# Kernel tuning notes

Hardware: AMD Instinct MI355X
Metric: run time of the kernel (lower is better)

The kernel has to match this reference:

```python
import jax, jax.numpy as jnp
import numpy as np

LAMBDA_COORD = 5.0
LAMBDA_NOOBJ = 0.5


def _iou(box1, box2):
    # boxes: [..., 4] in (cx, cy, w, h) format. Matches YoloLoss.IOU:
    # returns 0 when x_right < x_left or y_bottom < y_top (strict),
    # else intersection / (area1 + area2 - intersection).
    x1, y1, w1, h1 = box1[..., 0], box1[..., 1], box1[..., 2], box1[..., 3]
    x2, y2, w2, h2 = box2[..., 0], box2[..., 1], box2[..., 2], box2[..., 3]
    x_left = jnp.maximum(x1 - w1 / 2, x2 - w2 / 2)
    y_top = jnp.maximum(y1 - h1 / 2, y2 - h2 / 2)
    x_right = jnp.minimum(x1 + w1 / 2, x2 + w2 / 2)
    y_bottom = jnp.minimum(y1 + h1 / 2, y2 + h2 / 2)
    valid = jnp.logical_and(x_right >= x_left, y_bottom >= y_top)
    inter = (x_right - x_left) * (y_bottom - y_top)
    union = w1 * h1 + w2 * h2 - inter
    safe_union = jnp.where(union == 0, 1.0, union)
    return jnp.where(valid, inter / safe_union, 0.0)


def setup_inputs() -> dict:
    key = jax.random.key(0)
    k1, k2 = jax.random.split(key)
    B, S, D = 16384, 7, 30  # D = 2*5 + 20
    y = jax.random.normal(k1, (B, S, S, D), dtype=jnp.float32)
    gt = jax.random.normal(k2, (B, S, S, D), dtype=jnp.float32)
    return {"y": y, "gt": gt}


def reference(y, gt):
    pred, target = y, gt
    batch_size = pred.shape[0]
    obj = (target[..., 4] > 0).astype(pred.dtype)      # [B,S,S]
    noobj = (target[..., 4] == 0).astype(pred.dtype)   # [B,S,S]

    # class loss (mask over class channels, indices 10:)
    class_loss = jnp.sum(obj[..., None] * (target[..., 10:] - pred[..., 10:]) ** 2)

    # no-object confidence loss (channel 4, mask before responsibility edits)
    conf_loss_no_obj = jnp.sum(noobj * (target[..., 4] - pred[..., 4]) ** 2)

    # per-cell IOU of target box vs both predicted boxes
    tbox = target[..., 0:4]
    iou1 = _iou(tbox, pred[..., 0:4])   # [B,S,S]
    iou2 = _iou(tbox, pred[..., 5:9])   # [B,S,S]

    # responsibility: keep box1 iff iou1 > iou2 (ties -> box2), as in the torch loop
    resp1 = (iou1 > iou2).astype(pred.dtype)
    m1 = obj * resp1          # box1 responsible mask
    m2 = obj * (1.0 - resp1)  # box2 responsible mask

    # object confidence loss: confidence target is the IOU of the responsible box
    conf_loss_obj = jnp.sum(m1 * (iou1 - pred[..., 4]) ** 2
                            + m2 * (iou2 - pred[..., 9]) ** 2)

    # xy loss (channels 0,1 / 5,6)
    xy_loss = jnp.sum(m1 * ((target[..., 0] - pred[..., 0]) ** 2
                            + (target[..., 1] - pred[..., 1]) ** 2)
                      + m2 * ((target[..., 0] - pred[..., 5]) ** 2
                              + (target[..., 1] - pred[..., 6]) ** 2))

    # wh loss (channels 2,3 / 7,8)
    wh_loss = jnp.sum(m1 * ((target[..., 2] - pred[..., 2]) ** 2
                            + (target[..., 3] - pred[..., 3]) ** 2)
                      + m2 * ((target[..., 2] - pred[..., 7]) ** 2
                              + (target[..., 3] - pred[..., 8]) ** 2))

    total = (LAMBDA_COORD * xy_loss + LAMBDA_COORD * wh_loss
             + conf_loss_obj + LAMBDA_NOOBJ * conf_loss_no_obj
             + class_loss) / batch_size
    return total
```

## Files before the change

### kernel.cpp

```cpp
#include <hip/hip_runtime.h>

#define LAMBDA_COORD 5.0f
#define LAMBDA_NOOBJ 0.5f
#define DD 30
#define BLOCK 256
#define CPB 256
#define CHUNKS ((CPB * DD * 4) / 1024)

#define EL(A, k) (((k) & 1) ? A[(k) >> 1].y : A[(k) >> 1].x)

__device__ __forceinline__ float iou_t(float tx, float ty, float tw, float th,
                                       float px, float py, float pw, float ph) {
    float xl = fmaxf(tx - tw * 0.5f, px - pw * 0.5f);
    float yt = fmaxf(ty - th * 0.5f, py - ph * 0.5f);
    float xr = fminf(tx + tw * 0.5f, px + pw * 0.5f);
    float yb = fminf(ty + th * 0.5f, py + ph * 0.5f);
    bool valid = (xr >= xl) && (yb >= yt);
    float inter = (xr - xl) * (yb - yt);
    float uni = tw * th + pw * ph - inter;
    float safe = (uni == 0.0f) ? 1.0f : uni;
    return valid ? (inter / safe) : 0.0f;
}

__global__ __launch_bounds__(BLOCK, 2) void yolo_loss_kernel(
    const float* __restrict__ pred, const float* __restrict__ targ,
    float* __restrict__ out) {
    __shared__ __align__(16) float ldsP[CPB * DD];
    __shared__ __align__(16) float ldsT[CPB * DD];
    __shared__ float wpart[BLOCK / 64];

    const int tid  = threadIdx.x;
    const int lane = tid & 63;
    const int wv   = tid >> 6;

    const size_t base = (size_t)blockIdx.x * (CPB * DD);
    const float* gp = pred + base;
    const float* gt = targ + base;

    for (int s = wv; s < CHUNKS; s += BLOCK / 64) {
        __builtin_amdgcn_global_load_lds(
            (const __attribute__((address_space(1))) void*)(gp + s * 256 + lane * 4),
            (__attribute__((address_space(3))) void*)(ldsP + s * 256), 16, 0, 0);
        __builtin_amdgcn_global_load_lds(
            (const __attribute__((address_space(1))) void*)(gt + s * 256 + lane * 4),
            (__attribute__((address_space(3))) void*)(ldsT + s * 256), 16, 0, 0);
    }
    __syncthreads();

    const float2* lp = (const float2*)ldsP + tid * (DD / 2);
    const float2* lt = (const float2*)ldsT + tid * (DD / 2);

    float2 P[15], T[15];
#pragma unroll
    for (int j = 0; j < 15; ++j) P[j] = lp[j];
#pragma unroll
    for (int j = 0; j < 15; ++j) {
        if (j == 3 || j == 4) continue;
        T[j] = lt[j];
    }

    float t4 = EL(T, 4);
    float obj = (t4 > 0.0f) ? 1.0f : 0.0f;
    float noobj = (t4 == 0.0f) ? 1.0f : 0.0f;

    float cls = 0.0f;
#pragma unroll
    for (int j = 5; j < 15; ++j) {
        float dx = T[j].x - P[j].x;
        float dy = T[j].y - P[j].y;
        cls += dx * dx + dy * dy;
    }
    cls *= obj;

    float d4 = t4 - EL(P, 4);
    float conf_noobj = noobj * d4 * d4;

    float tx = EL(T, 0), ty = EL(T, 1), tw = EL(T, 2), th = EL(T, 3);
    float p0 = EL(P, 0), p1 = EL(P, 1), p2 = EL(P, 2), p3 = EL(P, 3);
    float p4 = EL(P, 4), p5 = EL(P, 5), p6 = EL(P, 6), p7 = EL(P, 7);
    float p8 = EL(P, 8), p9 = EL(P, 9);

    float iou1 = iou_t(tx, ty, tw, th, p0, p1, p2, p3);
    float iou2 = iou_t(tx, ty, tw, th, p5, p6, p7, p8);
    float resp1 = (iou1 > iou2) ? 1.0f : 0.0f;
    float m1 = obj * resp1;
    float m2 = obj * (1.0f - resp1);

    float e1 = iou1 - p4;
    float e2 = iou2 - p9;
    float conf_obj = m1 * e1 * e1 + m2 * e2 * e2;

    float dx1 = tx - p0, dy1 = ty - p1;
    float dx2 = tx - p5, dy2 = ty - p6;
    float xy = m1 * (dx1 * dx1 + dy1 * dy1) + m2 * (dx2 * dx2 + dy2 * dy2);

    float dw1 = tw - p2, dh1 = th - p3;
    float dw2 = tw - p7, dh2 = th - p8;
    float wh = m1 * (dw1 * dw1 + dh1 * dh1) + m2 * (dw2 * dw2 + dh2 * dh2);

    float loss = LAMBDA_COORD * (xy + wh) + conf_obj + LAMBDA_NOOBJ * conf_noobj + cls;

#pragma unroll
    for (int off = 32; off > 0; off >>= 1) loss += __shfl_down(loss, off);
    if ((tid & 63) == 0) wpart[tid >> 6] = loss;
    __syncthreads();
    if (tid == 0) {
        float s = wpart[0] + wpart[1] + wpart[2] + wpart[3];
        atomicAdd(out, s * (1.0f / 16384.0f));
    }
}

extern "C" void kernel_launch(void* const* d_in, const int* in_sizes, int n_in,
                              void* d_out, int out_size, void* d_ws, size_t ws_size,
                              hipStream_t stream) {
    const float* pred = (const float*)d_in[0];
    const float* targ = (const float*)d_in[1];
    float* out = (float*)d_out;

    hipMemsetAsync(out, 0, sizeof(float), stream);

    const int cells = in_sizes[0] / DD;
    const int grid = cells / CPB;
    yolo_loss_kernel<<<grid, BLOCK, 0, stream>>>(pred, targ, out);
}
```

Measured before the change: 207.2 us.

## Use persistent blocks with double-buffered async LDS staging of tiles

Replaces the one-tile-per-block launch with a fixed grid of 512 persistent 128-thread blocks. Each block loops over tiles and double-buffers them in LDS, so the next tile's global-to-LDS loads overlap compute on the current one. Per-tile results go into a register accumulator, leaving one atomic per block. This trades the occupancy of many resident blocks for explicit prefetch; with one block per CU launch bound and only 2 waves per block, in-flight memory may be lower.

```diff
diff --git a/kernel.cpp b/kernel.cpp
--- a/kernel.cpp
+++ b/kernel.cpp
@@ -3,9 +3,10 @@
 #define LAMBDA_COORD 5.0f
 #define LAMBDA_NOOBJ 0.5f
 #define DD 30
-#define BLOCK 256
-#define CPB 256
-#define CHUNKS ((CPB * DD * 4) / 1024)
+#define BLOCK 128
+#define CPB 128
+#define TILE_FLOATS (CPB * DD)
+#define GRID 512
 
 #define EL(A, k) (((k) & 1) ? A[(k) >> 1].y : A[(k) >> 1].x)
 
@@ -22,91 +23,116 @@
     return valid ? (inter / safe) : 0.0f;
 }
 
-__global__ __launch_bounds__(BLOCK, 2) void yolo_loss_kernel(
+__device__ __forceinline__ void stage_tile(const float* __restrict__ pred,
+                                           const float* __restrict__ targ,
+                                           size_t tile, float* buf,
+                                           int wv, int lane) {
+    const float* src = (wv ? targ : pred) + tile * (size_t)TILE_FLOATS + lane * 4;
+    float* dst = buf + wv * TILE_FLOATS;
+#pragma unroll
+    for (int c = 0; c < 15; ++c) {
+        __builtin_amdgcn_global_load_lds(
+            (const __attribute__((address_space(1))) void*)(src + c * 256),
+            (__attribute__((address_space(3))) void*)(dst + c * 256), 16, 0, 0);
+    }
+}
+
+#define WAIT_VM15() asm volatile("s_waitcnt vmcnt(15)" ::: "memory")
+#define WAIT_VM0()  asm volatile("s_waitcnt vmcnt(0)"  ::: "memory")
+
+__global__ __launch_bounds__(BLOCK, 1) void yolo_loss_kernel(
     const float* __restrict__ pred, const float* __restrict__ targ,
-    float* __restrict__ out) {
-    __shared__ __align__(16) float ldsP[CPB * DD];
-    __shared__ __align__(16) float ldsT[CPB * DD];
+    float* __restrict__ out, int n_tiles) {
+    __shared__ __align__(16) float lds[2][2 * TILE_FLOATS];
     __shared__ float wpart[BLOCK / 64];
 
     const int tid  = threadIdx.x;
     const int lane = tid & 63;
     const int wv   = tid >> 6;
+    const int b    = blockIdx.x;
 
-    const size_t base = (size_t)blockIdx.x * (CPB * DD);
-    const float* gp = pred + base;
-    const float* gt = targ + base;
+    const int my_tiles = (n_tiles - b + GRID - 1) / GRID;
 
-    for (int s = wv; s < CHUNKS; s += BLOCK / 64) {
-        __builtin_amdgcn_global_load_lds(
-            (const __attribute__((address_space(1))) void*)(gp + s * 256 + lane * 4),
-            (__attribute__((address_space(3))) void*)(ldsP + s * 256), 16, 0, 0);
-        __builtin_amdgcn_global_load_lds(
-            (const __attribute__((address_space(1))) void*)(gt + s * 256 + lane * 4),
-            (__attribute__((address_space(3))) void*)(ldsT + s * 256), 16, 0, 0);
-    }
-    __syncthreads();
+    stage_tile(pred, targ, (size_t)b, lds[0], wv, lane);
+    if (my_tiles > 1)
+        stage_tile(pred, targ, (size_t)b + GRID, lds[1], wv, lane);
 
-    const float2* lp = (const float2*)ldsP + tid * (DD / 2);
-    const float2* lt = (const float2*)ldsT + tid * (DD / 2);
+    float acc = 0.0f;
 
-    float2 P[15], T[15];
+    for (int k = 0; k < my_tiles; ++k) {
+        if (k + 1 < my_tiles) { WAIT_VM15(); } else { WAIT_VM0(); }
+        __builtin_amdgcn_s_barrier();
+        __builtin_amdgcn_sched_barrier(0);
+
+        const float* bufP = lds[k & 1];
+        const float* bufT = lds[k & 1] + TILE_FLOATS;
+        const float2* lp = (const float2*)bufP + tid * (DD / 2);
+        const float2* lt = (const float2*)bufT + tid * (DD / 2);
+
+        float2 P[15], T[15];
 #pragma unroll
-    for (int j = 0; j < 15; ++j) P[j] = lp[j];
+        for (int j = 0; j < 15; ++j) P[j] = lp[j];
 #pragma unroll
-    for (int j = 0; j < 15; ++j) {
-        if (j == 3 || j == 4) continue;
-        T[j] = lt[j];
+        for (int j = 0; j < 15; ++j) {
+            if (j == 3 || j == 4) continue;
+            T[j] = lt[j];
+        }
+
+        float t4 = EL(T, 4);
+        float obj = (t4 > 0.0f) ? 1.0f : 0.0f;
+        float noobj = (t4 == 0.0f) ? 1.0f : 0.0f;
+
+        float cls = 0.0f;
+#pragma unroll
+        for (int j = 5; j < 15; ++j) {
+            float dx = T[j].x - P[j].x;
+            float dy = T[j].y - P[j].y;
+            cls += dx * dx + dy * dy;
+        }
+        cls *= obj;
+
+        float d4 = t4 - EL(P, 4);
+        float conf_noobj = noobj * d4 * d4;
+
+        float tx = EL(T, 0), ty = EL(T, 1), tw = EL(T, 2), th = EL(T, 3);
+        float p0 = EL(P, 0), p1 = EL(P, 1), p2 = EL(P, 2), p3 = EL(P, 3);
+        float p4 = EL(P, 4), p5 = EL(P, 5), p6 = EL(P, 6), p7 = EL(P, 7);
+        float p8 = EL(P, 8), p9 = EL(P, 9);
+
+        float iou1 = iou_t(tx, ty, tw, th, p0, p1, p2, p3);
+        float iou2 = iou_t(tx, ty, tw, th, p5, p6, p7, p8);
+        float resp1 = (iou1 > iou2) ? 1.0f : 0.0f;
+        float m1 = obj * resp1;
+        float m2 = obj * (1.0f - resp1);
+
+        float e1 = iou1 - p4;
+        float e2 = iou2 - p9;
+        float conf_obj = m1 * e1 * e1 + m2 * e2 * e2;
+
+        float dx1 = tx - p0, dy1 = ty - p1;
+        float dx2 = tx - p5, dy2 = ty - p6;
+        float xy = m1 * (dx1 * dx1 + dy1 * dy1) + m2 * (dx2 * dx2 + dy2 * dy2);
+
+        float dw1 = tw - p2, dh1 = th - p3;
+        float dw2 = tw - p7, dh2 = th - p8;
+        float wh = m1 * (dw1 * dw1 + dh1 * dh1) + m2 * (dw2 * dw2 + dh2 * dh2);
+
+        acc += LAMBDA_COORD * (xy + wh) + conf_obj + LAMBDA_NOOBJ * conf_noobj + cls;
+
+        __builtin_amdgcn_s_barrier();
+        __builtin_amdgcn_sched_barrier(0);
+
+        if (k + 2 < my_tiles)
+            stage_tile(pred, targ, (size_t)b + (size_t)(k + 2) * GRID,
+                       lds[k & 1], wv, lane);
     }
 
-    float t4 = EL(T, 4);
-    float obj = (t4 > 0.0f) ? 1.0f : 0.0f;
-    float noobj = (t4 == 0.0f) ? 1.0f : 0.0f;
-
-    float cls = 0.0f;
 #pragma unroll
-    for (int j = 5; j < 15; ++j) {
-        float dx = T[j].x - P[j].x;
-        float dy = T[j].y - P[j].y;
-        cls += dx * dx + dy * dy;
-    }
-    cls *= obj;
-
-    float d4 = t4 - EL(P, 4);
-    float conf_noobj = noobj * d4 * d4;
-
-    float tx = EL(T, 0), ty = EL(T, 1), tw = EL(T, 2), th = EL(T, 3);
-    float p0 = EL(P, 0), p1 = EL(P, 1), p2 = EL(P, 2), p3 = EL(P, 3);
-    float p4 = EL(P, 4), p5 = EL(P, 5), p6 = EL(P, 6), p7 = EL(P, 7);
-    float p8 = EL(P, 8), p9 = EL(P, 9);
-
-    float iou1 = iou_t(tx, ty, tw, th, p0, p1, p2, p3);
-    float iou2 = iou_t(tx, ty, tw, th, p5, p6, p7, p8);
-    float resp1 = (iou1 > iou2) ? 1.0f : 0.0f;
-    float m1 = obj * resp1;
-    float m2 = obj * (1.0f - resp1);
-
-    float e1 = iou1 - p4;
-    float e2 = iou2 - p9;
-    float conf_obj = m1 * e1 * e1 + m2 * e2 * e2;
-
-    float dx1 = tx - p0, dy1 = ty - p1;
-    float dx2 = tx - p5, dy2 = ty - p6;
-    float xy = m1 * (dx1 * dx1 + dy1 * dy1) + m2 * (dx2 * dx2 + dy2 * dy2);
-
-    float dw1 = tw - p2, dh1 = th - p3;
-    float dw2 = tw - p7, dh2 = th - p8;
-    float wh = m1 * (dw1 * dw1 + dh1 * dh1) + m2 * (dw2 * dw2 + dh2 * dh2);
-
-    float loss = LAMBDA_COORD * (xy + wh) + conf_obj + LAMBDA_NOOBJ * conf_noobj + cls;
-
-#pragma unroll
-    for (int off = 32; off > 0; off >>= 1) loss += __shfl_down(loss, off);
-    if ((tid & 63) == 0) wpart[tid >> 6] = loss;
+    for (int off = 32; off > 0; off >>= 1) acc += __shfl_down(acc, off);
+    if (lane == 0) wpart[wv] = acc;
     __syncthreads();
     if (tid == 0) {
-        float s = wpart[0] + wpart[1] + wpart[2] + wpart[3];
-        atomicAdd(out, s * (1.0f / 16384.0f));
+        atomicAdd(out, (wpart[0] + wpart[1]) * (1.0f / 16384.0f));
     }
 }
 
@@ -120,6 +146,6 @@
     hipMemsetAsync(out, 0, sizeof(float), stream);
 
     const int cells = in_sizes[0] / DD;
-    const int grid = cells / CPB;
-    yolo_loss_kernel<<<grid, BLOCK, 0, stream>>>(pred, targ, out);
+    const int n_tiles = cells / CPB;
+    yolo_loss_kernel<<<GRID, BLOCK, 0, stream>>>(pred, targ, out, n_tiles);
 }
```

New measurement: 206.4 us. About the same (-0.4%).

## Halve block size and stage tiles via register float4 loads instead of direct-to-LDS

Applied to the files above, without the earlier changes.

Block and cells-per-block drop from 256 to 128, and the two LDS tiles become one contiguous buffer. The global_load_lds direct-to-LDS builtin is replaced by 15 float4 loads per thread into registers, followed by float4 stores to LDS. Each thread now reads from either the pred or the target tile depending on its index. The aims are more resident blocks per CU, since each block now uses about 30 KB of LDS, and more memory loads in flight per thread. The cost is more VGPRs and an extra register-to-LDS pass.

```diff
diff --git a/kernel.cpp b/kernel.cpp
--- a/kernel.cpp
+++ b/kernel.cpp
@@ -3,9 +3,9 @@
 #define LAMBDA_COORD 5.0f
 #define LAMBDA_NOOBJ 0.5f
 #define DD 30
-#define BLOCK 256
-#define CPB 256
-#define CHUNKS ((CPB * DD * 4) / 1024)
+#define BLOCK 128
+#define CPB 128
+#define TILE_FLOATS (CPB * DD)
 
 #define EL(A, k) (((k) & 1) ? A[(k) >> 1].y : A[(k) >> 1].x)
 
@@ -22,33 +22,34 @@
     return valid ? (inter / safe) : 0.0f;
 }
 
-__global__ __launch_bounds__(BLOCK, 2) void yolo_loss_kernel(
+__global__ __launch_bounds__(BLOCK) void yolo_loss_kernel(
     const float* __restrict__ pred, const float* __restrict__ targ,
     float* __restrict__ out) {
-    __shared__ __align__(16) float ldsP[CPB * DD];
-    __shared__ __align__(16) float ldsT[CPB * DD];
+    __shared__ __align__(16) float lds[2 * TILE_FLOATS];
     __shared__ float wpart[BLOCK / 64];
 
-    const int tid  = threadIdx.x;
-    const int lane = tid & 63;
-    const int wv   = tid >> 6;
+    const int tid = threadIdx.x;
 
-    const size_t base = (size_t)blockIdx.x * (CPB * DD);
-    const float* gp = pred + base;
-    const float* gt = targ + base;
+    const float* bp = pred + (size_t)blockIdx.x * TILE_FLOATS;
+    const float* bt = targ + (size_t)blockIdx.x * TILE_FLOATS;
 
-    for (int s = wv; s < CHUNKS; s += BLOCK / 64) {
-        __builtin_amdgcn_global_load_lds(
-            (const __attribute__((address_space(1))) void*)(gp + s * 256 + lane * 4),
-            (__attribute__((address_space(3))) void*)(ldsP + s * 256), 16, 0, 0);
-        __builtin_amdgcn_global_load_lds(
-            (const __attribute__((address_space(1))) void*)(gt + s * 256 + lane * 4),
-            (__attribute__((address_space(3))) void*)(ldsT + s * 256), 16, 0, 0);
+    float4 v[15];
+#pragma unroll
+    for (int c = 0; c < 15; ++c) {
+        int idx = c * BLOCK + tid;
+        const float* src = (idx < 960) ? (bp + (size_t)idx * 4)
+                                       : (bt + (size_t)(idx - 960) * 4);
+        v[c] = *(const float4*)src;
+    }
+#pragma unroll
+    for (int c = 0; c < 15; ++c) {
+        int idx = c * BLOCK + tid;
+        *(float4*)(lds + (size_t)idx * 4) = v[c];
     }
     __syncthreads();
 
-    const float2* lp = (const float2*)ldsP + tid * (DD / 2);
-    const float2* lt = (const float2*)ldsT + tid * (DD / 2);
+    const float2* lp = (const float2*)lds + tid * (DD / 2);
+    const float2* lt = (const float2*)(lds + TILE_FLOATS) + tid * (DD / 2);
 
     float2 P[15], T[15];
 #pragma unroll
@@ -105,8 +106,7 @@
     if ((tid & 63) == 0) wpart[tid >> 6] = loss;
     __syncthreads();
     if (tid == 0) {
-        float s = wpart[0] + wpart[1] + wpart[2] + wpart[3];
-        atomicAdd(out, s * (1.0f / 16384.0f));
+        atomicAdd(out, (wpart[0] + wpart[1]) * (1.0f / 16384.0f));
     }
 }
 
```

Result: slower. 230.4 us (+11.2%).
